# Optimization experiments

Hardware: AMD Instinct MI355X
Metric: run time of the kernel (lower is better)

## Reference

```python
import jax, jax.numpy as jnp
import numpy as np

R = 4        # in_transformations == out_transformations
FS = 3       # filter_size
PAD = 1
STRIDE = 1


def setup_inputs() -> dict:
    key = jax.random.key(0)
    k1, k2, k3 = jax.random.split(key, 3)
    B, Cin, O, K = 16, 64, 64, 4
    Ctot = Cin * R  # 256
    x = jax.random.normal(k1, (B, Ctot, 64, 64), dtype=jnp.float32)
    # kernel bank: [num_dynamic_kernels, out_channels, in_channels, f, f]
    kernel_bank = jax.random.normal(k2, (K, O, Cin, FS, FS), dtype=jnp.float32) * 0.05
    # routing fc: Linear(total_in_channels -> num_kernels)
    fc_w = jax.random.normal(k3, (K, Ctot), dtype=jnp.float32) * 0.05
    fc_b = jnp.zeros((K,), dtype=jnp.float32)
    return {"x": x, "kernel_bank": kernel_bank, "fc_w": fc_w, "fc_b": fc_b}


def reference(x, kernel_bank, fc_w, fc_b):
    B, Ctot, H, W = x.shape
    K, O, Cin, f, _ = kernel_bank.shape
    # --- dynamic routing: global avg pool -> fc -> sigmoid ---
    pooled = x.mean(axis=(2, 3))                                  # [B, Ctot]
    coeffs = jax.nn.sigmoid(pooled @ fc_w.T + fc_b)               # [B, K]
    # --- per-sample kernel synthesis ---
    base = jnp.einsum('bk,kocij->bocij', coeffs, kernel_bank)     # [B, O, Cin, f, f]
    # rotations rot90^k for k in 0..R-1 (matches torch.rot90 dims=(-2,-1))
    rotated = jnp.stack([jnp.rot90(base, k, axes=(-2, -1)) for k in range(R)], axis=1)  # [B, R, O, Cin, f, f]
    # block kernel: block (r_out, r_in) uses rotation index (r_out - r_in) % R,
    # so the r_in sum of convs becomes one conv over all R*Cin input channels.
    r_out = jnp.arange(R)[:, None]
    r_in = jnp.arange(R)[None, :]
    idx = (r_out - r_in) % R                                      # [R, R]
    big = rotated[:, idx]                                         # [B, R_out, R_in, O, Cin, f, f]
    big = big.transpose(0, 1, 3, 2, 4, 5, 6).reshape(B, R * O, R * Cin, f, f)
    # --- per-sample conv (vmapped over batch; each sample has its own kernel) ---
    def conv_one(xi, wi):
        return jax.lax.conv_general_dilated(
            xi[None], wi,
            window_strides=(STRIDE, STRIDE),
            padding=[(PAD, PAD), (PAD, PAD)],
            dimension_numbers=('NCHW', 'OIHW', 'NCHW'))[0]
    return jax.vmap(conv_one)(x, big)                             # [B, R*O, H, W]
```

## Files before the change

kernel.cpp:

```cpp
#include <hip/hip_runtime.h>
#include <hip/hip_bf16.h>
#include <math.h>

#define BATCH 16
#define CT    256
#define HW    64
#define OCH   64
#define NK    4
#define HP    66
#define NPIX  4356

typedef __attribute__((ext_vector_type(4)))  float  f32x4;
typedef __attribute__((ext_vector_type(8)))  short  s16x8;
typedef __attribute__((ext_vector_type(4)))  unsigned short u16x4;

#define GLOBAL_AS __attribute__((address_space(1)))
#define LDS_AS    __attribute__((address_space(3)))

__device__ __constant__ int c_rotsrc[4][9] = {
    {0,1,2,3,4,5,6,7,8},
    {2,5,8,1,4,7,0,3,6},
    {8,7,6,5,4,3,2,1,0},
    {6,3,0,7,4,1,8,5,2}
};

static __device__ inline unsigned short f2bf(float f) {
    union { __hip_bfloat16 h; unsigned short u; } cv;
    cv.h = __float2bfloat16(f);
    return cv.u;
}

__global__ __launch_bounds__(256) void xpose_pool(const float* __restrict__ x,
                                                  unsigned short* __restrict__ xTg,
                                                  float* __restrict__ partial) {
    const int ci0 = blockIdx.x * 64;
    const int ch0 = ci0 >> 5;
    const int pr  = blockIdx.y;
    const int b   = blockIdx.z;
    const int t   = threadIdx.x;

    if (pr == 0 || pr == HP-1) {
        for (int u = t; u < 528; u += 256) {
            int chl = (u >= 264) ? 1 : 0;
            int rem = u - chl*264;
            int c = rem >> 2, q = rem & 3;
            *(s16x8*)(xTg + (((size_t)(b*8 + ch0 + chl))*NPIX + pr*HP + c)*32 + q*8) =
                (s16x8)(short)0;
        }
        return;
    }
    const int r = pr - 1;

    __shared__ unsigned short tile[64][70];
    const int cilH = t >> 4;
    const int c0   = (t & 15) * 4;
    #pragma unroll
    for (int i = 0; i < 4; ++i) {
        int cil = cilH + i*16;
        f32x4 v = *(const f32x4*)(x + (((size_t)(b*CT + ci0 + cil))*HW + r)*HW + c0);
        tile[cil][c0+0] = f2bf(v[0]);
        tile[cil][c0+1] = f2bf(v[1]);
        tile[cil][c0+2] = f2bf(v[2]);
        tile[cil][c0+3] = f2bf(v[3]);
        float s = v[0] + v[1] + v[2] + v[3];
        s += __shfl_xor(s, 1, 16);
        s += __shfl_xor(s, 2, 16);
        s += __shfl_xor(s, 4, 16);
        s += __shfl_xor(s, 8, 16);
        if ((t & 15) == 0)
            partial[((size_t)(b*HW) + r)*CT + ci0 + cil] = s;
    }
    __syncthreads();

    if (t < 16) {
        int side = t >> 3, r8 = t & 7;
        int chl = r8 >> 2, q = r8 & 3;
        *(s16x8*)(xTg + (((size_t)(b*8 + ch0 + chl))*NPIX + pr*HP + side*(HP-1))*32 + q*8) =
            (s16x8)(short)0;
    }
    #pragma unroll
    for (int i = 0; i < 4; ++i) {
        const int chl = i >> 1;
        const int c   = (i & 1)*32 + (t >> 3);
        const int q   = t & 7;
        u16x4 w;
        w[0] = tile[chl*32 + q*4 + 0][c];
        w[1] = tile[chl*32 + q*4 + 1][c];
        w[2] = tile[chl*32 + q*4 + 2][c];
        w[3] = tile[chl*32 + q*4 + 3][c];
        *(u16x4*)(xTg + (((size_t)(b*8 + ch0 + chl))*NPIX + pr*HP + c + 1)*32 + q*4) = w;
    }
}

__global__ __launch_bounds__(256) void coeff_kernel(const float* __restrict__ partial,
                                                    const float* __restrict__ fc_w,
                                                    const float* __restrict__ fc_b,
                                                    float* __restrict__ coeffs) {
    const int b = blockIdx.x;
    const int t = threadIdx.x;
    const float* pp = partial + (size_t)b*HW*CT + t;
    float s = 0.f;
    #pragma unroll 8
    for (int r = 0; r < HW; ++r) s += pp[(size_t)r*CT];
    __shared__ float pool[CT];
    pool[t] = s * (1.f / (HW*HW));
    __syncthreads();
    const int w = t >> 6, l = t & 63;
    float d = 0.f;
    for (int c = l; c < CT; c += 64) d += pool[c] * fc_w[w*CT + c];
    for (int off = 32; off; off >>= 1) d += __shfl_down(d, off, 64);
    if (l == 0)
        coeffs[b*NK + w] = 1.f / (1.f + expf(-(d + fc_b[w])));
}

__global__ __launch_bounds__(256) void bankrot_kernel(const float* __restrict__ bank,
                                                      float* __restrict__ P) {
    const int idx = blockIdx.x * 256 + threadIdx.x;
    const int o = idx & 63;
    const int c = (idx >> 6) & 63;
    const int k = idx >> 12;
    const float* bp = bank + ((size_t)((k*OCH + o)*64 + c))*9;
    float v[9];
    #pragma unroll
    for (int s = 0; s < 9; ++s) v[s] = bp[s];
    #pragma unroll
    for (int rr = 0; rr < 4; ++rr)
        #pragma unroll
        for (int s = 0; s < 9; ++s)
            P[(size_t)(((k*4 + rr)*9 + s))*4096 + c*64 + o] = v[c_rotsrc[rr][s]];
}

__global__ __launch_bounds__(256) void wbuild_kernel(const float* __restrict__ coeffs,
                                                     const float* __restrict__ P,
                                                     unsigned short* __restrict__ Wb) {
    const int cig = blockIdx.x;
    const int s   = blockIdx.y;
    const int co  = threadIdx.x;
    const int ro  = co >> 6;
    const int o   = co & 63;
    const int ri  = cig >> 3;
    const int rr  = (ro - ri) & 3;
    const int c8  = (cig & 7) * 8;

    float r[NK][8];
    #pragma unroll
    for (int k = 0; k < NK; ++k) {
        const float* pp = P + (size_t)(((k*4 + rr)*9 + s))*4096 + o;
        #pragma unroll
        for (int q = 0; q < 8; ++q)
            r[k][q] = pp[(c8 + q)*64];
    }
    #pragma unroll
    for (int b = 0; b < BATCH; ++b) {
        const float cf0 = coeffs[b*NK+0], cf1 = coeffs[b*NK+1];
        const float cf2 = coeffs[b*NK+2], cf3 = coeffs[b*NK+3];
        s16x8 w;
        #pragma unroll
        for (int q = 0; q < 8; ++q) {
            float v = cf0*r[0][q] + cf1*r[1][q] + cf2*r[2][q] + cf3*r[3][q];
            w[q] = (short)f2bf(v);
        }
        *(s16x8*)(Wb + ((((size_t)(b*9 + s)*32 + cig)*256 + co) << 3)) = w;
    }
}

#define CHUNK_U 1056
#define BUF_U   1088
#define MF(A_, B_, C_) __builtin_amdgcn_mfma_f32_16x16x32_bf16(A_, B_, C_, 0, 0, 0)

__global__ __launch_bounds__(128, 2) void conv_mfma(
        const unsigned short* __restrict__ xTg,
        const unsigned short* __restrict__ Wb,
        float* __restrict__ out) {
    const int bid  = blockIdx.x;
    const int b    = (bid & 7)*2 + ((bid >> 3) & 1);
    const int rest = bid >> 4;
    const int coT  = rest & 1;
    const int r0   = (rest >> 1) * 2;

    const int t    = threadIdx.x;
    const int w    = t >> 6;
    const int lane = t & 63;
    const int lo16 = lane & 15;
    const int hi4  = lane >> 4;

    __shared__ __align__(16) unsigned short Xs[2*BUF_U*8];

    f32x4 acc[4][8];
    #pragma unroll
    for (int f = 0; f < 4; ++f)
        #pragma unroll
        for (int p = 0; p < 8; ++p)
            acc[f][p] = (f32x4)0.f;

    const unsigned short* Wlane = Wb +
        (((size_t)(b*9*32) + hi4)*256 + coT*128 + w*64 + lo16)*8;

#define LOADA(DST, CH, S)                                                       \
    do {                                                                        \
        const unsigned short* wp = Wlane + (size_t)((S)*32 + (CH)*4)*2048;      \
        _Pragma("unroll")                                                       \
        for (int f_ = 0; f_ < 4; ++f_)                                          \
            DST[f_] = *(const s16x8*)(wp + f_*128);                             \
    } while (0)

#define STAGE(CH, BUF)                                                          \
    do {                                                                        \
        const unsigned short* srcb = xTg +                                      \
            (((size_t)(b*8 + (CH)))*NPIX + r0*HP)*32;                           \
        _Pragma("unroll")                                                       \
        for (int it = 0; it < 9; ++it) {                                        \
            int ubase = it*128 + w*64;                                          \
            if (ubase < CHUNK_U) {                                              \
                int u  = ubase + lane;                                          \
                int us = u > (CHUNK_U-1) ? (CHUNK_U-1) : u;  \
                __builtin_amdgcn_global_load_lds(                               \
                    (const GLOBAL_AS void*)(srcb + (size_t)us*8),               \
                    (LDS_AS void*)(Xs + (size_t)((BUF)*BUF_U + ubase)*8),       \
                    16, 0, 0);                                                  \
            }                                                                   \
        }                                                                       \
    } while (0)

    STAGE(0, 0);
    __syncthreads();

    for (int ch = 0; ch < 8; ++ch) {
        s16x8 A[9][4];
        LOADA(A[0], ch, 0);
        LOADA(A[1], ch, 1);
        LOADA(A[2], ch, 2);
        __builtin_amdgcn_sched_barrier(0);
        if (ch < 7) STAGE(ch+1, (ch+1) & 1);

        const char* Xb = (const char*)Xs + (ch & 1)*(BUF_U*16)
                         + lo16*64 + hi4*16;

        #pragma unroll
        for (int s = 0; s < 9; ++s) {
            if (s < 6) LOADA(A[s+3], ch, s+3);
            const int dr = s/3, dc = s%3;
            #pragma unroll
            for (int p = 0; p < 8; ++p) {
                const int pix = ((p>>2) + dr)*HP + dc + (p&3)*16;
                s16x8 bf = *(const s16x8*)(Xb + pix*64);
                acc[0][p] = MF(A[s][0], bf, acc[0][p]);
                acc[1][p] = MF(A[s][1], bf, acc[1][p]);
                acc[2][p] = MF(A[s][2], bf, acc[2][p]);
                acc[3][p] = MF(A[s][3], bf, acc[3][p]);
            }
        }
        __syncthreads();
    }
#undef STAGE
#undef LOADA

    #pragma unroll
    for (int f = 0; f < 4; ++f)
        #pragma unroll
        for (int p = 0; p < 8; ++p) {
            const int row  = r0 + (p >> 2);
            const int colb = (p & 3)*16 + lo16;
            #pragma unroll
            for (int j = 0; j < 4; ++j) {
                int co = coT*128 + w*64 + f*16 + hi4*4 + j;
                out[(((size_t)(b*CT + co))*HW + row)*HW + colb] = acc[f][p][j];
            }
        }
}

extern "C" void kernel_launch(void* const* d_in, const int* in_sizes, int n_in,
                              void* d_out, int out_size, void* d_ws, size_t ws_size,
                              hipStream_t stream) {
    const float* x    = (const float*)d_in[0];
    const float* bank = (const float*)d_in[1];
    const float* fc_w = (const float*)d_in[2];
    const float* fc_b = (const float*)d_in[3];
    float* out = (float*)d_out;

    char* wsb = (char*)d_ws;
    float* partial = (float*)wsb;
    float* Prot    = (float*)wsb;
    float* coeffs  = (float*)(wsb + 2359296);
    unsigned short* Wb  = (unsigned short*)(wsb + 2360320);
    unsigned short* xTg = (unsigned short*)(wsb + 21234688);

    xpose_pool<<<dim3(4, HP, BATCH), 256, 0, stream>>>(x, xTg, partial);
    coeff_kernel<<<BATCH, 256, 0, stream>>>(partial, fc_w, fc_b, coeffs);
    bankrot_kernel<<<64, 256, 0, stream>>>(bank, Prot);
    wbuild_kernel<<<dim3(32, 9), 256, 0, stream>>>(coeffs, Prot, Wb);
    conv_mfma<<<1024, 128, 0, stream>>>(xTg, Wb, out);
}
```

Measured before the change: 95.64 us.

## Split conv into single-wave blocks with unbuffered per-wave LDS staging

After: 97.27 us. Within noise of the previous version (+1.7%).

```diff
diff --git a/kernel.cpp b/kernel.cpp
--- a/kernel.cpp
+++ b/kernel.cpp
@@ -168,23 +168,21 @@
 #define BUF_U   1088
 #define MF(A_, B_, C_) __builtin_amdgcn_mfma_f32_16x16x32_bf16(A_, B_, C_, 0, 0, 0)
 
-__global__ __launch_bounds__(128, 2) void conv_mfma(
+__global__ __launch_bounds__(64, 2) void conv_mfma(
         const unsigned short* __restrict__ xTg,
         const unsigned short* __restrict__ Wb,
         float* __restrict__ out) {
     const int bid  = blockIdx.x;
     const int b    = (bid & 7)*2 + ((bid >> 3) & 1);
     const int rest = bid >> 4;
-    const int coT  = rest & 1;
-    const int r0   = (rest >> 1) * 2;
-
-    const int t    = threadIdx.x;
-    const int w    = t >> 6;
-    const int lane = t & 63;
+    const int coq  = rest & 3;
+    const int r0   = (rest >> 2) * 2;
+
+    const int lane = threadIdx.x;
     const int lo16 = lane & 15;
     const int hi4  = lane >> 4;
 
-    __shared__ __align__(16) unsigned short Xs[2*BUF_U*8];
+    __shared__ __align__(16) unsigned short Xs[BUF_U*8];
 
     f32x4 acc[4][8];
     #pragma unroll
@@ -194,7 +192,7 @@
             acc[f][p] = (f32x4)0.f;
 
     const unsigned short* Wlane = Wb +
-        (((size_t)(b*9*32) + hi4)*256 + coT*128 + w*64 + lo16)*8;
+        (((size_t)(b*9*32) + hi4)*256 + coq*64 + lo16)*8;
 
 #define LOADA(DST, CH, S)                                                       \
     do {                                                                        \
@@ -204,41 +202,36 @@
             DST[f_] = *(const s16x8*)(wp + f_*128);                             \
     } while (0)
 
-#define STAGE(CH, BUF)                                                          \
+#define STAGE(CH)                                                               \
     do {                                                                        \
         const unsigned short* srcb = xTg +                                      \
             (((size_t)(b*8 + (CH)))*NPIX + r0*HP)*32;                           \
         _Pragma("unroll")                                                       \
-        for (int it = 0; it < 9; ++it) {                                        \
-            int ubase = it*128 + w*64;                                          \
-            if (ubase < CHUNK_U) {                                              \
-                int u  = ubase + lane;                                          \
-                int us = u > (CHUNK_U-1) ? (CHUNK_U-1) : u;  \
-                __builtin_amdgcn_global_load_lds(                               \
-                    (const GLOBAL_AS void*)(srcb + (size_t)us*8),               \
-                    (LDS_AS void*)(Xs + (size_t)((BUF)*BUF_U + ubase)*8),       \
-                    16, 0, 0);                                                  \
-            }                                                                   \
+        for (int it = 0; it < 17; ++it) {                                       \
+            int ubase = it*64;                                                  \
+            int u  = ubase + lane;                                              \
+            int us = u > (CHUNK_U-1) ? (CHUNK_U-1) : u;      \
+            __builtin_amdgcn_global_load_lds(                                   \
+                (const GLOBAL_AS void*)(srcb + (size_t)us*8),                   \
+                (LDS_AS void*)(Xs + (size_t)ubase*8),                           \
+                16, 0, 0);                                                      \
         }                                                                       \
     } while (0)
-
-    STAGE(0, 0);
-    __syncthreads();
 
     for (int ch = 0; ch < 8; ++ch) {
         s16x8 A[9][4];
         LOADA(A[0], ch, 0);
         LOADA(A[1], ch, 1);
-        LOADA(A[2], ch, 2);
+        asm volatile("s_waitcnt lgkmcnt(0)" ::: "memory");
+        STAGE(ch);
+        asm volatile("s_waitcnt vmcnt(0)" ::: "memory");
         __builtin_amdgcn_sched_barrier(0);
-        if (ch < 7) STAGE(ch+1, (ch+1) & 1);
-
-        const char* Xb = (const char*)Xs + (ch & 1)*(BUF_U*16)
-                         + lo16*64 + hi4*16;
+
+        const char* Xb = (const char*)Xs + lo16*64 + hi4*16;
 
         #pragma unroll
         for (int s = 0; s < 9; ++s) {
-            if (s < 6) LOADA(A[s+3], ch, s+3);
+            if (s < 7) LOADA(A[s+2], ch, s+2);
             const int dr = s/3, dc = s%3;
             #pragma unroll
             for (int p = 0; p < 8; ++p) {
@@ -250,7 +243,6 @@
                 acc[3][p] = MF(A[s][3], bf, acc[3][p]);
             }
         }
-        __syncthreads();
     }
 #undef STAGE
 #undef LOADA
@@ -263,7 +255,7 @@
             const int colb = (p & 3)*16 + lo16;
             #pragma unroll
             for (int j = 0; j < 4; ++j) {
-                int co = coT*128 + w*64 + f*16 + hi4*4 + j;
+                int co = coq*64 + f*16 + hi4*4 + j;
                 out[(((size_t)(b*CT + co))*HW + row)*HW + colb] = acc[f][p][j];
             }
         }
@@ -289,5 +281,5 @@
     coeff_kernel<<<BATCH, 256, 0, stream>>>(partial, fc_w, fc_b, coeffs);
     bankrot_kernel<<<64, 256, 0, stream>>>(bank, Prot);
     wbuild_kernel<<<dim3(32, 9), 256, 0, stream>>>(coeffs, Prot, Wb);
-    conv_mfma<<<1024, 128, 0, stream>>>(xTg, Wb, out);
-}
+    conv_mfma<<<2048, 64, 0, stream>>>(xTg, Wb, out);
+}
```
